# Kernel optimization log

Hardware: AMD Instinct MI355X
Metric: run time of the kernel (lower is better)

The kernel has to match this reference:

```python
import jax, jax.numpy as jnp
import numpy as np

IN_C, OUT_C, K = 32, 32, 3
PAD = 1


def setup_inputs() -> dict:
    key = jax.random.key(0)
    kx, kw, kb = jax.random.split(key, 3)
    x = jax.random.normal(kx, (16, IN_C, 256, 256), dtype=jnp.float32)
    # Kaiming-ish init scale for the conv weight, matching nn.Conv2d defaults roughly
    fan_in = IN_C * K * K
    w = jax.random.normal(kw, (OUT_C, IN_C, K, K), dtype=jnp.float32) / np.sqrt(fan_in)
    b = jax.random.normal(kb, (OUT_C,), dtype=jnp.float32) * 0.01
    return {"x": x, "weight": w, "bias": b}


def reference(x, weight, bias):
    # Faithful math of SparseConv2d.forward: the block-sparse Triton path computes
    # the same result as a dense conv (zero blocks contribute zero), so the
    # reference is a standard 3x3 stride-1 pad-1 conv, NCHW / OIHW layout.
    y = jax.lax.conv_general_dilated(
        x, weight,
        window_strides=(1, 1),
        padding=((PAD, PAD), (PAD, PAD)),
        dimension_numbers=("NCHW", "OIHW", "NCHW"),
    )
    return y + bias[None, :, None, None]
```

## Files before the change

### kernel.cpp

```cpp
#include <hip/hip_runtime.h>


constexpr int N_  = 16;
constexpr int C_  = 32;
constexpr int OC_ = 32;
constexpr int H_  = 256;
constexpr int W_  = 256;

constexpr int XSTR = 20;
constexpr int XROW = 258 * XSTR;
constexpr int WSTRD = 36;

typedef __attribute__((ext_vector_type(4)))  short short4v;
typedef __attribute__((ext_vector_type(8)))  short short8v;
typedef __attribute__((ext_vector_type(16))) float float16v;

static __device__ __forceinline__ unsigned short f2bf(float f) {
    unsigned int u = __float_as_uint(f);
    unsigned int r = (u + 0x7FFFu + ((u >> 16) & 1u)) >> 16;
    return (unsigned short)r;
}

static __device__ __forceinline__ unsigned pk2(float a, float b) {
    return (unsigned)f2bf(a) | ((unsigned)f2bf(b) << 16);
}

static __device__ __forceinline__ short8v load8(const unsigned short* p) {
    short4v lo = *(const short4v*)p;
    short4v hi = *(const short4v*)(p + 4);
    return __builtin_shufflevector(lo, hi, 0, 1, 2, 3, 4, 5, 6, 7);
}

__global__ __launch_bounds__(256, 3) void conv3x3_mfma_kernel(
    const float* __restrict__ x,
    const float* __restrict__ wgt,
    const float* __restrict__ bias,
    float* __restrict__ out)
{
    __shared__ __align__(16) unsigned short ldsX[3 * XROW];
    __shared__ __align__(16) unsigned short ldsW[9 * 32 * WSTRD];

    const int tid = threadIdx.x;

    const int id = blockIdx.x;
    const int L  = (id & 7) * 512 + (id >> 3);
    const int n  = L >> 8;
    const int h  = L & (H_ - 1);

    for (int i = tid; i < OC_ * C_ * 9; i += 256) {
        const float v = wgt[i];
        const int oc  = i / 288;
        const int rem = i - oc * 288;
        const int ic  = rem / 9;
        const int t9  = rem - ic * 9;
        ldsW[(t9 * 32 + oc) * WSTRD + ic] = f2bf(v);
    }

    const int lane = tid & 63;
    const int wv   = tid >> 6;
    const int col  = lane & 31;
    const int qd   = lane >> 5;

    float16v acc0, acc1;
    #pragma unroll
    for (int r = 0; r < 16; ++r) {
        const float bv = bias[(r & 3) + 8 * (r >> 2) + 4 * qd];
        acc0[r] = bv;
        acc1[r] = bv;
    }

    const int wlo = tid & 31;
    const int icp = tid >> 5;
    const int w0a = wv * 64;
    const int w0b = wv * 64 + 32;

    for (int half = 0; half < 2; ++half) {
        if (half) __syncthreads();

        const int icg = half * 16 + 2 * icp;
        #pragma unroll
        for (int r = 0; r < 3; ++r) {
            const int hy = h + r - 1;
            unsigned short* dst = &ldsX[r * XROW];
            if (hy >= 0 && hy < H_) {
                const float* p0 = x + (((size_t)(n * C_ + icg) * H_ + hy) * W_);
                const float* p1 = p0 + (size_t)H_ * W_;
                #pragma unroll
                for (int wb = 0; wb < 4; ++wb) {
                    const int w = wb * 64 + 2 * wlo;
                    const float2 a = *(const float2*)(p0 + w);
                    const float2 b = *(const float2*)(p1 + w);
                    *(unsigned*)&dst[(w + 1) * XSTR + 2 * icp] = pk2(a.x, b.x);
                    *(unsigned*)&dst[(w + 2) * XSTR + 2 * icp] = pk2(a.y, b.y);
                }
            } else {
                #pragma unroll
                for (int wb = 0; wb < 4; ++wb) {
                    const int w = wb * 64 + 2 * wlo;
                    *(unsigned*)&dst[(w + 1) * XSTR + 2 * icp] = 0u;
                    *(unsigned*)&dst[(w + 2) * XSTR + 2 * icp] = 0u;
                }
            }
        }
        if (tid < 24) {
            const int r  = tid >> 3;
            const int q  = tid & 7;
            const int wi = (q & 4) ? 257 : 0;
            const int c  = q & 3;
            *(unsigned long long*)&ldsX[r * XROW + wi * XSTR + c * 4] = 0ull;
        }
        __syncthreads();

        #pragma unroll
        for (int kh = 0; kh < 3; ++kh) {
            #pragma unroll
            for (int kw = 0; kw < 3; ++kw) {
                const int t9 = kh * 3 + kw;
                const short8v av =
                    load8(&ldsW[(t9 * 32 + col) * WSTRD + half * 16 + qd * 8]);
                const short8v b0 =
                    load8(&ldsX[kh * XROW + (w0a + col + kw) * XSTR + qd * 8]);
                const short8v b1 =
                    load8(&ldsX[kh * XROW + (w0b + col + kw) * XSTR + qd * 8]);
                acc0 = __builtin_amdgcn_mfma_f32_32x32x16_bf16(av, b0, acc0, 0, 0, 0);
                acc1 = __builtin_amdgcn_mfma_f32_32x32x16_bf16(av, b1, acc1, 0, 0, 0);
            }
        }
    }

    float* outp = out + (size_t)n * OC_ * H_ * W_ + (size_t)h * W_;
    #pragma unroll
    for (int r = 0; r < 16; ++r) {
        const int oc = (r & 3) + 8 * (r >> 2) + 4 * qd;
        outp[(size_t)oc * H_ * W_ + w0a + col] = acc0[r];
        outp[(size_t)oc * H_ * W_ + w0b + col] = acc1[r];
    }
}

extern "C" void kernel_launch(void* const* d_in, const int* in_sizes, int n_in,
                              void* d_out, int out_size, void* d_ws, size_t ws_size,
                              hipStream_t stream) {
    const float* x    = (const float*)d_in[0];
    const float* wgt  = (const float*)d_in[1];
    const float* bias = (const float*)d_in[2];
    float* out        = (float*)d_out;

    dim3 grid(N_ * H_);
    dim3 block(256);
    conv3x3_mfma_kernel<<<grid, block, 0, stream>>>(x, wgt, bias, out);
}
```

Measured before the change: 262.0 us.

## Prepack bf16 weights once and prefetch next input half during MFMA

A small pre-kernel now converts and re-lays-out the weights into bf16 in workspace once, instead of every block doing the conversion with integer divides. Blocks instead copy the prepacked tile with 16-byte loads. The second channel half's input rows are loaded into registers while the first half's MFMAs run. Packing uses the hardware bf16 pack instruction, and output stores are nontemporal. The cost is higher register pressure from the prefetch buffers and an extra kernel launch.

```diff
diff --git a/kernel.cpp b/kernel.cpp
--- a/kernel.cpp
+++ b/kernel.cpp
@@ -10,6 +10,8 @@
 constexpr int XSTR = 20;
 constexpr int XROW = 258 * XSTR;
 constexpr int WSTRD = 36;
+constexpr int WELEMS = 9 * 32 * WSTRD;
+constexpr int WBYTES = WELEMS * 2;
 
 typedef __attribute__((ext_vector_type(4)))  short short4v;
 typedef __attribute__((ext_vector_type(8)))  short short8v;
@@ -21,8 +23,10 @@
     return (unsigned short)r;
 }
 
-static __device__ __forceinline__ unsigned pk2(float a, float b) {
-    return (unsigned)f2bf(a) | ((unsigned)f2bf(b) << 16);
+static __device__ __forceinline__ unsigned cvtpk(float lo, float hi) {
+    unsigned r;
+    asm("v_cvt_pk_bf16_f32 %0, %1, %2" : "=v"(r) : "v"(lo), "v"(hi));
+    return r;
 }
 
 static __device__ __forceinline__ short8v load8(const unsigned short* p) {
@@ -31,14 +35,28 @@
     return __builtin_shufflevector(lo, hi, 0, 1, 2, 3, 4, 5, 6, 7);
 }
 
+__global__ void conv_w_prep(const float* __restrict__ wgt,
+                            unsigned short* __restrict__ wp) {
+    const int i = blockIdx.x * 256 + threadIdx.x;
+    if (i >= OC_ * C_ * 9) return;
+    const float v = wgt[i];
+    const int oc  = i / 288;
+    const int rem = i - oc * 288;
+    const int ic  = rem / 9;
+    const int t9  = rem - ic * 9;
+    wp[(t9 * 32 + oc) * WSTRD + ic] = f2bf(v);
+}
+
+template<bool USE_WS>
 __global__ __launch_bounds__(256, 3) void conv3x3_mfma_kernel(
     const float* __restrict__ x,
     const float* __restrict__ wgt,
     const float* __restrict__ bias,
+    const unsigned short* __restrict__ wpk,
     float* __restrict__ out)
 {
     __shared__ __align__(16) unsigned short ldsX[3 * XROW];
-    __shared__ __align__(16) unsigned short ldsW[9 * 32 * WSTRD];
+    __shared__ __align__(16) unsigned short ldsW[WELEMS];
 
     const int tid = threadIdx.x;
 
@@ -47,19 +65,61 @@
     const int n  = L >> 8;
     const int h  = L & (H_ - 1);
 
-    for (int i = tid; i < OC_ * C_ * 9; i += 256) {
-        const float v = wgt[i];
-        const int oc  = i / 288;
-        const int rem = i - oc * 288;
-        const int ic  = rem / 9;
-        const int t9  = rem - ic * 9;
-        ldsW[(t9 * 32 + oc) * WSTRD + ic] = f2bf(v);
-    }
-
     const int lane = tid & 63;
     const int wv   = tid >> 6;
     const int col  = lane & 31;
     const int qd   = lane >> 5;
+    const int wlo  = tid & 31;
+    const int icp  = tid >> 5;
+    const int w0a  = wv * 64;
+    const int w0b  = wv * 64 + 32;
+    const size_t HW = (size_t)H_ * W_;
+
+    float2 pa[3][4], pb[3][4];
+    auto load_half = [&](int half, float2 (&ra)[3][4], float2 (&rb)[3][4]) {
+        const int icg = half * 16 + 2 * icp;
+        const float* base = x + (size_t)(n * C_ + icg) * HW;
+        #pragma unroll
+        for (int r = 0; r < 3; ++r) {
+            const int hy = h + r - 1;
+            if (hy >= 0 && hy < H_) {
+                const float* p0 = base + (size_t)hy * W_;
+                const float* p1 = p0 + HW;
+                #pragma unroll
+                for (int wb = 0; wb < 4; ++wb) {
+                    const int w = wb * 64 + 2 * wlo;
+                    ra[r][wb] = *(const float2*)(p0 + w);
+                    rb[r][wb] = *(const float2*)(p1 + w);
+                }
+            } else {
+                #pragma unroll
+                for (int wb = 0; wb < 4; ++wb) {
+                    ra[r][wb] = make_float2(0.f, 0.f);
+                    rb[r][wb] = make_float2(0.f, 0.f);
+                }
+            }
+        }
+    };
+    load_half(0, pa, pb);
+
+    if (USE_WS) {
+        const int4* src = (const int4*)wpk;
+        int4* dst = (int4*)&ldsW[0];
+        #pragma unroll
+        for (int i2 = 0; i2 < 6; ++i2) {
+            const int idx = tid + i2 * 256;
+            if (idx < WBYTES / 16) dst[idx] = src[idx];
+        }
+    } else {
+        for (int i = tid; i < OC_ * C_ * 9; i += 256) {
+            const float v = wgt[i];
+            const int oc  = i / 288;
+            const int rem = i - oc * 288;
+            const int ic  = rem / 9;
+            const int t9  = rem - ic * 9;
+            ldsW[(t9 * 32 + oc) * WSTRD + ic] = f2bf(v);
+        }
+    }
 
     float16v acc0, acc1;
     #pragma unroll
@@ -69,48 +129,20 @@
         acc1[r] = bv;
     }
 
-    const int wlo = tid & 31;
-    const int icp = tid >> 5;
-    const int w0a = wv * 64;
-    const int w0b = wv * 64 + 32;
-
-    for (int half = 0; half < 2; ++half) {
-        if (half) __syncthreads();
-
-        const int icg = half * 16 + 2 * icp;
+    auto write_half = [&](float2 (&ra)[3][4], float2 (&rb)[3][4]) {
         #pragma unroll
         for (int r = 0; r < 3; ++r) {
-            const int hy = h + r - 1;
             unsigned short* dst = &ldsX[r * XROW];
-            if (hy >= 0 && hy < H_) {
-                const float* p0 = x + (((size_t)(n * C_ + icg) * H_ + hy) * W_);
-                const float* p1 = p0 + (size_t)H_ * W_;
-                #pragma unroll
-                for (int wb = 0; wb < 4; ++wb) {
-                    const int w = wb * 64 + 2 * wlo;
-                    const float2 a = *(const float2*)(p0 + w);
-                    const float2 b = *(const float2*)(p1 + w);
-                    *(unsigned*)&dst[(w + 1) * XSTR + 2 * icp] = pk2(a.x, b.x);
-                    *(unsigned*)&dst[(w + 2) * XSTR + 2 * icp] = pk2(a.y, b.y);
-                }
-            } else {
-                #pragma unroll
-                for (int wb = 0; wb < 4; ++wb) {
-                    const int w = wb * 64 + 2 * wlo;
-                    *(unsigned*)&dst[(w + 1) * XSTR + 2 * icp] = 0u;
-                    *(unsigned*)&dst[(w + 2) * XSTR + 2 * icp] = 0u;
-                }
+            #pragma unroll
+            for (int wb = 0; wb < 4; ++wb) {
+                const int w = wb * 64 + 2 * wlo;
+                *(unsigned*)&dst[(w + 1) * XSTR + 2 * icp] = cvtpk(ra[r][wb].x, rb[r][wb].x);
+                *(unsigned*)&dst[(w + 2) * XSTR + 2 * icp] = cvtpk(ra[r][wb].y, rb[r][wb].y);
             }
         }
-        if (tid < 24) {
-            const int r  = tid >> 3;
-            const int q  = tid & 7;
-            const int wi = (q & 4) ? 257 : 0;
-            const int c  = q & 3;
-            *(unsigned long long*)&ldsX[r * XROW + wi * XSTR + c * 4] = 0ull;
-        }
-        __syncthreads();
-
+    };
+
+    auto mfma_half = [&](int half) {
         #pragma unroll
         for (int kh = 0; kh < 3; ++kh) {
             #pragma unroll
@@ -126,14 +158,32 @@
                 acc1 = __builtin_amdgcn_mfma_f32_32x32x16_bf16(av, b1, acc1, 0, 0, 0);
             }
         }
-    }
-
-    float* outp = out + (size_t)n * OC_ * H_ * W_ + (size_t)h * W_;
+    };
+
+    write_half(pa, pb);
+    if (tid < 24) {
+        const int r  = tid >> 3;
+        const int q  = tid & 7;
+        const int wi = (q & 4) ? 257 : 0;
+        const int c  = q & 3;
+        *(unsigned long long*)&ldsX[r * XROW + wi * XSTR + c * 4] = 0ull;
+    }
+    __syncthreads();
+
+    load_half(1, pa, pb);
+    mfma_half(0);
+    __syncthreads();
+
+    write_half(pa, pb);
+    __syncthreads();
+    mfma_half(1);
+
+    float* outp = out + (size_t)n * OC_ * HW + (size_t)h * W_;
     #pragma unroll
     for (int r = 0; r < 16; ++r) {
         const int oc = (r & 3) + 8 * (r >> 2) + 4 * qd;
-        outp[(size_t)oc * H_ * W_ + w0a + col] = acc0[r];
-        outp[(size_t)oc * H_ * W_ + w0b + col] = acc1[r];
+        __builtin_nontemporal_store(acc0[r], &outp[(size_t)oc * HW + w0a + col]);
+        __builtin_nontemporal_store(acc1[r], &outp[(size_t)oc * HW + w0b + col]);
     }
 }
 
@@ -147,5 +197,12 @@
 
     dim3 grid(N_ * H_);
     dim3 block(256);
-    conv3x3_mfma_kernel<<<grid, block, 0, stream>>>(x, wgt, bias, out);
-}
+
+    if (d_ws != nullptr && ws_size >= (size_t)WBYTES) {
+        unsigned short* wp = (unsigned short*)d_ws;
+        conv_w_prep<<<dim3(36), dim3(256), 0, stream>>>(wgt, wp);
+        conv3x3_mfma_kernel<true><<<grid, block, 0, stream>>>(x, wgt, bias, wp, out);
+    } else {
+        conv3x3_mfma_kernel<false><<<grid, block, 0, stream>>>(x, wgt, bias, nullptr, out);
+    }
+}
```

After: 245.1 us. 6.4% less time.

## Drop LDS staging; load input taps directly from global and prepack weights

Applied to the files above, without the earlier changes.

Removes the shared-memory staging of input rows and weights. Each lane now gathers its 3x3 neighbourhood straight from global memory, relying on L1/L2 for reuse, and converts it with the hardware bf16 pack instruction. Weights are pre-converted to packed bf16 fragments by a separate prep kernel into workspace. The grid doubles so each wave computes one 32-column MFMA tile instead of two. This trades LDS traffic and barriers for many more scalar, strided global loads per MFMA, plus an extra kernel launch.

```diff
diff --git a/kernel.cpp b/kernel.cpp
--- a/kernel.cpp
+++ b/kernel.cpp
@@ -6,134 +6,148 @@
 constexpr int OC_ = 32;
 constexpr int H_  = 256;
 constexpr int W_  = 256;
+constexpr int HW_ = H_ * W_;
 
-constexpr int XSTR = 20;
-constexpr int XROW = 258 * XSTR;
-constexpr int WSTRD = 36;
+constexpr int WGROUPS = 36 * 32;
+constexpr int WBYTES  = WGROUPS * 16;
 
-typedef __attribute__((ext_vector_type(4)))  short short4v;
 typedef __attribute__((ext_vector_type(8)))  short short8v;
+typedef __attribute__((ext_vector_type(4)))  int   int4v;
 typedef __attribute__((ext_vector_type(16))) float float16v;
 
-static __device__ __forceinline__ unsigned short f2bf(float f) {
-    unsigned int u = __float_as_uint(f);
-    unsigned int r = (u + 0x7FFFu + ((u >> 16) & 1u)) >> 16;
-    return (unsigned short)r;
+static __device__ __forceinline__ unsigned cvtpk(float lo, float hi) {
+    unsigned r;
+    asm("v_cvt_pk_bf16_f32 %0, %1, %2" : "=v"(r) : "v"(lo), "v"(hi));
+    return r;
 }
 
-static __device__ __forceinline__ unsigned pk2(float a, float b) {
-    return (unsigned)f2bf(a) | ((unsigned)f2bf(b) << 16);
+static __device__ __forceinline__ short8v pack8(float v0, float v1, float v2, float v3,
+                                                float v4, float v5, float v6, float v7) {
+    int4v iv;
+    iv.x = (int)cvtpk(v0, v1);
+    iv.y = (int)cvtpk(v2, v3);
+    iv.z = (int)cvtpk(v4, v5);
+    iv.w = (int)cvtpk(v6, v7);
+    return __builtin_bit_cast(short8v, iv);
 }
 
-static __device__ __forceinline__ short8v load8(const unsigned short* p) {
-    short4v lo = *(const short4v*)p;
-    short4v hi = *(const short4v*)(p + 4);
-    return __builtin_shufflevector(lo, hi, 0, 1, 2, 3, 4, 5, 6, 7);
+__global__ void conv_w_prep(const float* __restrict__ wgt,
+                            unsigned* __restrict__ wp) {
+    const int g = blockIdx.x * 256 + threadIdx.x;
+    if (g >= WGROUPS) return;
+    const int oc  = g & 31;
+    const int q   = g >> 5;
+    const int qd  = q & 1;
+    const int hf  = (q >> 1) & 1;
+    const int t9  = q >> 2;
+    const int icb = hf * 16 + qd * 8;
+    float v[8];
+    #pragma unroll
+    for (int j = 0; j < 8; ++j) v[j] = wgt[(oc * 32 + icb + j) * 9 + t9];
+    wp[g * 4 + 0] = cvtpk(v[0], v[1]);
+    wp[g * 4 + 1] = cvtpk(v[2], v[3]);
+    wp[g * 4 + 2] = cvtpk(v[4], v[5]);
+    wp[g * 4 + 3] = cvtpk(v[6], v[7]);
 }
 
-__global__ __launch_bounds__(256, 3) void conv3x3_mfma_kernel(
+template<bool USE_WS>
+__global__ __launch_bounds__(256) void conv3x3_mfma_kernel(
     const float* __restrict__ x,
     const float* __restrict__ wgt,
     const float* __restrict__ bias,
+    const unsigned* __restrict__ wpk,
     float* __restrict__ out)
 {
-    __shared__ __align__(16) unsigned short ldsX[3 * XROW];
-    __shared__ __align__(16) unsigned short ldsW[9 * 32 * WSTRD];
-
     const int tid = threadIdx.x;
 
     const int id = blockIdx.x;
-    const int L  = (id & 7) * 512 + (id >> 3);
-    const int n  = L >> 8;
-    const int h  = L & (H_ - 1);
-
-    for (int i = tid; i < OC_ * C_ * 9; i += 256) {
-        const float v = wgt[i];
-        const int oc  = i / 288;
-        const int rem = i - oc * 288;
-        const int ic  = rem / 9;
-        const int t9  = rem - ic * 9;
-        ldsW[(t9 * 32 + oc) * WSTRD + ic] = f2bf(v);
-    }
+    const int L  = (id & 7) * 1024 + (id >> 3);
+    const int n  = L >> 9;
+    const int r9 = L & 511;
+    const int h  = r9 >> 1;
+    const int side = r9 & 1;
 
     const int lane = tid & 63;
     const int wv   = tid >> 6;
     const int col  = lane & 31;
     const int qd   = lane >> 5;
+    const int w0   = side * 128 + wv * 32;
+    const int wc   = w0 + col;
 
-    float16v acc0, acc1;
+    const int  left0  = (wc == 0)      ? 1 : 0;
+    const int  right0 = (wc == W_ - 1) ? -1 : 0;
+    const bool mL = (wc > 0);
+    const bool mR = (wc < W_ - 1);
+
+    float16v acc;
     #pragma unroll
-    for (int r = 0; r < 16; ++r) {
-        const float bv = bias[(r & 3) + 8 * (r >> 2) + 4 * qd];
-        acc0[r] = bv;
-        acc1[r] = bv;
-    }
+    for (int r = 0; r < 16; ++r)
+        acc[r] = bias[(r & 3) + 8 * (r >> 2) + 4 * qd];
 
-    const int wlo = tid & 31;
-    const int icp = tid >> 5;
-    const int w0a = wv * 64;
-    const int w0b = wv * 64 + 32;
+    const unsigned bidx = (unsigned)(n * C_ * HW_ + h * W_ + wc);
 
-    for (int half = 0; half < 2; ++half) {
-        if (half) __syncthreads();
-
-        const int icg = half * 16 + 2 * icp;
-        #pragma unroll
-        for (int r = 0; r < 3; ++r) {
-            const int hy = h + r - 1;
-            unsigned short* dst = &ldsX[r * XROW];
-            if (hy >= 0 && hy < H_) {
-                const float* p0 = x + (((size_t)(n * C_ + icg) * H_ + hy) * W_);
-                const float* p1 = p0 + (size_t)H_ * W_;
+    #pragma unroll
+    for (int hf = 0; hf < 2; ++hf) {
+        short8v af[9];
+        if (USE_WS) {
+            #pragma unroll
+            for (int t9 = 0; t9 < 9; ++t9) {
+                const int g = ((t9 * 2 + hf) * 2 + qd) * 32 + col;
+                af[t9] = __builtin_bit_cast(short8v,
+                             *(const int4v*)(wpk + (size_t)g * 4));
+            }
+        } else {
+            const int icb = hf * 16 + qd * 8;
+            #pragma unroll
+            for (int t9 = 0; t9 < 9; ++t9) {
+                float v[8];
                 #pragma unroll
-                for (int wb = 0; wb < 4; ++wb) {
-                    const int w = wb * 64 + 2 * wlo;
-                    const float2 a = *(const float2*)(p0 + w);
-                    const float2 b = *(const float2*)(p1 + w);
-                    *(unsigned*)&dst[(w + 1) * XSTR + 2 * icp] = pk2(a.x, b.x);
-                    *(unsigned*)&dst[(w + 2) * XSTR + 2 * icp] = pk2(a.y, b.y);
-                }
-            } else {
-                #pragma unroll
-                for (int wb = 0; wb < 4; ++wb) {
-                    const int w = wb * 64 + 2 * wlo;
-                    *(unsigned*)&dst[(w + 1) * XSTR + 2 * icp] = 0u;
-                    *(unsigned*)&dst[(w + 2) * XSTR + 2 * icp] = 0u;
-                }
+                for (int j = 0; j < 8; ++j)
+                    v[j] = wgt[(col * 32 + icb + j) * 9 + t9];
+                af[t9] = pack8(v[0], v[1], v[2], v[3], v[4], v[5], v[6], v[7]);
             }
         }
-        if (tid < 24) {
-            const int r  = tid >> 3;
-            const int q  = tid & 7;
-            const int wi = (q & 4) ? 257 : 0;
-            const int c  = q & 3;
-            *(unsigned long long*)&ldsX[r * XROW + wi * XSTR + c * 4] = 0ull;
-        }
-        __syncthreads();
+
+        unsigned vo[8];
+        #pragma unroll
+        for (int j = 0; j < 8; ++j)
+            vo[j] = bidx + (unsigned)((hf * 16 + qd * 8 + j) * HW_);
 
         #pragma unroll
         for (int kh = 0; kh < 3; ++kh) {
+            if (kh == 0 && h == 0)      continue;
+            if (kh == 2 && h == H_ - 1) continue;
             #pragma unroll
             for (int kw = 0; kw < 3; ++kw) {
-                const int t9 = kh * 3 + kw;
-                const short8v av =
-                    load8(&ldsW[(t9 * 32 + col) * WSTRD + half * 16 + qd * 8]);
-                const short8v b0 =
-                    load8(&ldsX[kh * XROW + (w0a + col + kw) * XSTR + qd * 8]);
-                const short8v b1 =
-                    load8(&ldsX[kh * XROW + (w0b + col + kw) * XSTR + qd * 8]);
-                acc0 = __builtin_amdgcn_mfma_f32_32x32x16_bf16(av, b0, acc0, 0, 0, 0);
-                acc1 = __builtin_amdgcn_mfma_f32_32x32x16_bf16(av, b1, acc1, 0, 0, 0);
+                const int abias = (kw == 0) ? 1 : ((kw == 2) ? -1 : 0);
+                float bv[8];
+                #pragma unroll
+                for (int j = 0; j < 8; ++j) {
+                    const float* p = x + vo[j]
+                        + ((kw == 0) ? left0 : ((kw == 2) ? right0 : 0));
+                    bv[j] = p[(kh - 1) * W_ + (kw - 1)];
+                }
+                if (kw == 0) {
+                    #pragma unroll
+                    for (int j = 0; j < 8; ++j) bv[j] = mL ? bv[j] : 0.f;
+                } else if (kw == 2) {
+                    #pragma unroll
+                    for (int j = 0; j < 8; ++j) bv[j] = mR ? bv[j] : 0.f;
+                }
+                (void)abias;
+                const short8v bf = pack8(bv[0], bv[1], bv[2], bv[3],
+                                         bv[4], bv[5], bv[6], bv[7]);
+                acc = __builtin_amdgcn_mfma_f32_32x32x16_bf16(
+                          af[kh * 3 + kw], bf, acc, 0, 0, 0);
             }
         }
     }
 
-    float* outp = out + (size_t)n * OC_ * H_ * W_ + (size_t)h * W_;
+    const size_t outb = (size_t)n * OC_ * HW_ + (size_t)h * W_ + wc;
     #pragma unroll
     for (int r = 0; r < 16; ++r) {
         const int oc = (r & 3) + 8 * (r >> 2) + 4 * qd;
-        outp[(size_t)oc * H_ * W_ + w0a + col] = acc0[r];
-        outp[(size_t)oc * H_ * W_ + w0b + col] = acc1[r];
+        out[outb + (size_t)oc * HW_] = acc[r];
     }
 }
 
@@ -145,7 +159,14 @@
     const float* bias = (const float*)d_in[2];
     float* out        = (float*)d_out;
 
-    dim3 grid(N_ * H_);
+    dim3 grid(N_ * H_ * 2);
     dim3 block(256);
-    conv3x3_mfma_kernel<<<grid, block, 0, stream>>>(x, wgt, bias, out);
+
+    if (d_ws != nullptr && ws_size >= (size_t)WBYTES) {
+        unsigned* wp = (unsigned*)d_ws;
+        conv_w_prep<<<dim3(5), dim3(256), 0, stream>>>(wgt, wp);
+        conv3x3_mfma_kernel<true><<<grid, block, 0, stream>>>(x, wgt, bias, wp, out);
+    } else {
+        conv3x3_mfma_kernel<false><<<grid, block, 0, stream>>>(x, wgt, bias, nullptr, out);
+    }
 }
```

New measurement: 289.5 us. 10.5% more time.
